# Kernel tuning notes

Measured on AMD Instinct MI355X. Metric: run time of the kernel, lower is better.

Reference implementation:

```python
import jax, jax.numpy as jnp
import numpy as np

Z, K, H, B = 32, 4, 128, 32768  # z_size, num_flows, h_size, batch


def setup_inputs() -> dict:
    key = jax.random.key(0)
    ks = jax.random.split(key, 12)
    s = 0.05  # weight scale so tanh stays in informative range
    return {
        "z0": jax.random.normal(ks[0], (B, Z), jnp.float32),
        "h": jax.random.normal(ks[1], (B, H), jnp.float32),
        "Wd": jax.random.normal(ks[2], (K * Z * Z, H), jnp.float32) * s,
        "bd": jax.random.normal(ks[3], (K * Z * Z,), jnp.float32) * s,
        "Wd1": jax.random.normal(ks[4], (K * Z, H), jnp.float32) * s,
        "bd1": jax.random.normal(ks[5], (K * Z,), jnp.float32) * s,
        "Wd2": jax.random.normal(ks[6], (K * Z, H), jnp.float32) * s,
        "bd2": jax.random.normal(ks[7], (K * Z,), jnp.float32) * s,
        "Wb": jax.random.normal(ks[8], (K * Z, H), jnp.float32) * s,
        "bb": jax.random.normal(ks[9], (K * Z,), jnp.float32) * s,
        "is_test": 0,
    }


def _encode(h, Wd, bd, Wd1, bd1, Wd2, bd2, Wb, bb):
    bsz = h.shape[0]
    full_d = (h @ Wd.T + bd).reshape(bsz, Z, Z, K)
    diag1 = jnp.tanh(h @ Wd1.T + bd1).reshape(bsz, Z, K)
    diag2 = jnp.tanh(h @ Wd2.T + bd2).reshape(bsz, Z, K)
    triu = jnp.triu(jnp.ones((Z, Z), full_d.dtype), 1)[None, :, :, None]
    eye = jnp.eye(Z, dtype=full_d.dtype)[None, :, :, None]
    # r1: strictly-upper of full_d with learned tanh diagonal; r2: transpose analog
    r1 = full_d * triu + eye * diag1[:, :, None, :]
    r2 = jnp.transpose(full_d, (0, 2, 1, 3)) * triu + eye * diag2[:, :, None, :]
    b = (h @ Wb.T + bb).reshape(bsz, Z, K)
    return r1, r2, b, diag1, diag2


def reference(z0, h, Wd, bd, Wd1, bd1, Wd2, bd2, Wb, bb, is_test):
    r1, r2, b, diag1, diag2 = _encode(h, Wd, bd, Wd1, bd1, Wd2, bd2, Wb, bb)
    z = z0
    log_det_j = jnp.zeros(z0.shape[0], z0.dtype)
    for k in range(K):
        r1k, r2k, bk = r1[..., k], r2[..., k], b[..., k]
        flip = (k % 2 == 1)  # alternate permutation (reversal) / identity
        z_per = z[:, ::-1] if flip else z
        pre = jnp.einsum('bi,bji->bj', z_per, r2k) + bk  # z_per @ r2^T + b
        t = jnp.tanh(pre)
        dz = jnp.einsum('bj,bij->bi', t, r1k)            # tanh(.) @ r1^T
        if flip:
            dz = dz[:, ::-1]
        z = z + dz
        # |det| = prod_i |1 + tanh'(pre_i) * diag_r1_i * diag_r2_i|
        diag_j = (1.0 - t * t) * (diag1[:, :, k] * diag2[:, :, k]) + 1.0
        log_det_j = log_det_j + jnp.sum(jnp.log(jnp.abs(diag_j)), axis=-1)
    return z, log_det_j
```

## Files before the change

### kernel.cpp

```cpp
#include <hip/hip_runtime.h>

typedef unsigned short ushort_t;
typedef unsigned int uint_t;
typedef __attribute__((ext_vector_type(8))) _Float16 f16x8;
typedef __attribute__((ext_vector_type(4))) _Float16 f16x4;
typedef __attribute__((ext_vector_type(4))) float floatx4;

#define ZDIM 32
#define KDIM 4
#define HDIM 128
#define B_TOTAL 32768
#define TB 64

#define WS_WD16 0
#define WS_SM16 524288

#define D_PJ 68
#define D_BI 2180
#define SH_D_OFF 0
#define AUX_PITCH 132
#define AUX_MS (64 * AUX_PITCH)
#define SH_AUX_OFF 0
#define SH_H_OFF 101376
#define SH_ZT_OFF 139520
#define SH_TT_OFF 148224
#define LDS_BYTES 152576

__device__ __forceinline__ float fast_tanh(float x) {
    float e = __expf(2.0f * x);
    return 1.0f - 2.0f / (e + 1.0f);
}
__device__ __forceinline__ float f16lo(uint_t v) {
    return (float)__builtin_bit_cast(_Float16, (ushort_t)(v & 0xFFFFu));
}
__device__ __forceinline__ float f16hi(uint_t v) {
    return (float)__builtin_bit_cast(_Float16, (ushort_t)(v >> 16));
}
__device__ __forceinline__ ushort_t f2h(float x) {
    return __builtin_bit_cast(ushort_t, (_Float16)x);
}
__device__ __forceinline__ ushort4 cvt4(float4 v) {
    ushort4 o; o.x = f2h(v.x); o.y = f2h(v.y); o.z = f2h(v.z); o.w = f2h(v.w);
    return o;
}
__device__ __forceinline__ uint2 packq(const float* p) {
    uint2 r;
    r.x = (uint_t)f2h(p[0]) | ((uint_t)f2h(p[1]) << 16);
    r.y = (uint_t)f2h(p[2]) | ((uint_t)f2h(p[3]) << 16);
    return r;
}
__device__ __forceinline__ float half_at(uint2 q, int kk) {
    uint_t w = (kk & 2) ? q.y : q.x;
    return (kk & 1) ? f16hi(w) : f16lo(w);
}

__global__ __launch_bounds__(256) void convert_kernel(
    const float* __restrict__ Wd, const float* __restrict__ Wd1,
    const float* __restrict__ Wd2, const float* __restrict__ Wb,
    ushort_t* __restrict__ ws)
{
    int g = blockIdx.x * 256 + threadIdx.x;
    if (g < 131072) {
        int k = g >> 15;
        int rem = g & 32767;
        int n = rem >> 5;
        int c4 = rem & 31;
        float4 v = *((const float4*)Wd + (size_t)(4 * n + k) * 32 + c4);
        ((ushort4*)(ws + WS_WD16))[g] = cvt4(v);
    } else {
        int s = g - 131072;
        const float* src = (s < 4096) ? Wd1 : ((s < 8192) ? Wd2 : Wb);
        int r = s & 4095;
        float4 v = ((const float4*)src)[r];
        ((ushort4*)(ws + WS_SM16))[s] = cvt4(v);
    }
}

__global__ __launch_bounds__(512, 2) void sylv_kernel(
    const ushort_t* __restrict__ wsb,
    const float* __restrict__ hglob,
    const float* __restrict__ z0,
    const float* __restrict__ bd,
    const float* __restrict__ bd1,
    const float* __restrict__ bd2,
    const float* __restrict__ bb,
    float* __restrict__ out)
{
    extern __shared__ char smem[];
    _Float16* Dh     = (_Float16*)(smem + SH_D_OFF);
    float*    sh_aux = (float*)(smem + SH_AUX_OFF);
    _Float16* sh_h   = (_Float16*)(smem + SH_H_OFF);
    float*    sh_zt  = (float*)(smem + SH_ZT_OFF);
    _Float16* Th     = (_Float16*)(smem + SH_TT_OFF);

    const int t   = threadIdx.x;
    const int bg0 = blockIdx.x * TB;
    const int lane = t & 63, w = t >> 6;
    const int l15 = lane & 15, l4 = lane >> 4;
    const int fj = t & 31;
    const int fg = t >> 5;

    {
        const float4* hsrc = (const float4*)(hglob + (size_t)bg0 * HDIM);
        #pragma unroll
        for (int it = 0; it < 4; ++it) {
            int c = t + it * 512;
            int row = c >> 5, col4 = c & 31;
            float4 v = hsrc[c];
            *(ushort4*)((ushort_t*)sh_h + row * 136 + col4 * 4) = cvt4(v);
        }
        int zb = t >> 3;
        int zi0 = (t & 7) * 4;
        float4 zv = *(const float4*)(z0 + (size_t)(bg0 + zb) * ZDIM + zi0);
        sh_zt[(zi0 + 0) * 68 + zb] = zv.x;
        sh_zt[(zi0 + 1) * 68 + zb] = zv.y;
        sh_zt[(zi0 + 2) * 68 + zb] = zv.z;
        sh_zt[(zi0 + 3) * 68 + zb] = zv.w;
    }
    __syncthreads();

    f16x8 ah[4][4];
    #pragma unroll
    for (int mt = 0; mt < 4; ++mt)
        #pragma unroll
        for (int kc = 0; kc < 4; ++kc)
            ah[mt][kc] = *(const f16x8*)(sh_h + (mt * 16 + l15) * 136 + kc * 32 + l4 * 8);

    #pragma unroll 1
    for (int pi = 0; pi < 3; ++pi) {
        int p = w * 3 + pi;
        int m_i = p >> 3, nt = p & 7, n = nt * 16 + l15;
        const _Float16* wp = (const _Float16*)(wsb + WS_SM16) + (size_t)(m_i * 128 + n) * 128 + l4 * 8;
        floatx4 a[4];
        #pragma unroll
        for (int mt = 0; mt < 4; ++mt) a[mt] = (floatx4){0.f, 0.f, 0.f, 0.f};
        #pragma unroll
        for (int kc = 0; kc < 4; ++kc) {
            f16x8 bh = *(const f16x8*)(wp + kc * 32);
            #pragma unroll
            for (int mt = 0; mt < 4; ++mt)
                a[mt] = __builtin_amdgcn_mfma_f32_16x16x32_f16(ah[mt][kc], bh, a[mt], 0, 0, 0);
        }
        const float* bv = (m_i == 0) ? bd1 : ((m_i == 1) ? bd2 : bb);
        float bias = bv[n];
        float* ap = sh_aux + m_i * AUX_MS + n;
        #pragma unroll
        for (int mt = 0; mt < 4; ++mt) {
            #pragma unroll
            for (int r = 0; r < 4; ++r) {
                float v0 = a[mt][r] + bias;
                if (m_i < 2) v0 = fast_tanh(v0);
                ap[(mt * 16 + l4 * 4 + r) * AUX_PITCH] = v0;
            }
        }
    }
    __syncthreads();

    uint2 d1q[4], d2q[4], bpq[4];
    {
        #pragma unroll
        for (int e = 0; e < 4; ++e) {
            const float* base = sh_aux + (4 * fg + e) * AUX_PITCH + 4 * fj;
            d1q[e] = packq(base + 0 * AUX_MS);
            d2q[e] = packq(base + 1 * AUX_MS);
            bpq[e] = packq(base + 2 * AUX_MS);
        }
    }
    __syncthreads();

    float ld4[4] = {0.f, 0.f, 0.f, 0.f};

    #pragma unroll 1
    for (int kk = 0; kk < KDIM; ++kk) {
        const _Float16* wdk = (const _Float16*)(wsb + WS_WD16) + (size_t)kk * 131072;
        #pragma unroll 2
        for (int g = 0; g < 8; ++g) {
            int nc = w * 128 + g * 16 + l15;
            const _Float16* w0 = wdk + (size_t)nc * 128 + l4 * 8;
            floatx4 a[4];
            #pragma unroll
            for (int mt = 0; mt < 4; ++mt) a[mt] = (floatx4){0.f, 0.f, 0.f, 0.f};
            #pragma unroll
            for (int kc = 0; kc < 4; ++kc) {
                f16x8 b0 = *(const f16x8*)(w0 + kc * 32);
                #pragma unroll
                for (int mt = 0; mt < 4; ++mt)
                    a[mt] = __builtin_amdgcn_mfma_f32_16x16x32_f16(ah[mt][kc], b0, a[mt], 0, 0, 0);
            }
            int ii = nc >> 5, jj = nc & 31;
            int base = ii * D_BI + jj * D_PJ;
            float bias0 = bd[4 * nc + kk];
            #pragma unroll
            for (int mt = 0; mt < 4; ++mt) {
                f16x4 o;
                #pragma unroll
                for (int r = 0; r < 4; ++r)
                    o[r] = (_Float16)(a[mt][r] + bias0);
                *(f16x4*)(Dh + base + mt * 16 + l4 * 4) = o;
            }
        }
        __syncthreads();

        {
            const bool flip = (kk & 1) != 0;
            const int zr_j = flip ? (31 - fj) : fj;

            float s4[4];
            {
                floatx4 zj = *(const floatx4*)(sh_zt + zr_j * 68 + 4 * fg);
                #pragma unroll
                for (int e = 0; e < 4; ++e)
                    s4[e] = half_at(bpq[e], kk) + zj[e] * half_at(d2q[e], kk);
            }
            #pragma unroll 4
            for (int i = 0; i < 32; ++i) {
                int zr_i = flip ? (31 - i) : i;
                floatx4 zi4 = *(const floatx4*)(sh_zt + zr_i * 68 + 4 * fg);
                f16x4 dd = *(const f16x4*)(Dh + i * D_BI + fj * D_PJ + 4 * fg);
                bool gt = (i > fj);
                #pragma unroll
                for (int e = 0; e < 4; ++e)
                    s4[e] = fmaf((float)dd[e], gt ? zi4[e] : 0.0f, s4[e]);
            }
            float tq4[4];
            {
                f16x4 tth;
                #pragma unroll
                for (int e = 0; e < 4; ++e) {
                    float tt = fast_tanh(s4[e]);
                    tq4[e] = tt;
                    tth[e] = (_Float16)tt;
                    float d1 = half_at(d1q[e], kk), d2 = half_at(d2q[e], kk);
                    ld4[e] += __logf(fabsf((1.f - tt * tt) * (d1 * d2) + 1.f));
                }
                *(f16x4*)(Th + fj * 68 + 4 * fg) = tth;
            }
            asm volatile("s_waitcnt lgkmcnt(0)" ::: "memory");

            float dzv4[4];
            #pragma unroll
            for (int e = 0; e < 4; ++e)
                dzv4[e] = tq4[e] * half_at(d1q[e], kk);
            #pragma unroll 4
            for (int j2 = 0; j2 < 32; ++j2) {
                f16x4 tt4 = *(const f16x4*)(Th + j2 * 68 + 4 * fg);
                f16x4 dd  = *(const f16x4*)(Dh + fj * D_BI + j2 * D_PJ + 4 * fg);
                bool gt = (j2 > fj);
                #pragma unroll
                for (int e = 0; e < 4; ++e)
                    dzv4[e] = fmaf((float)dd[e], gt ? (float)tt4[e] : 0.0f, dzv4[e]);
            }
            float* zp = sh_zt + zr_j * 68 + 4 * fg;
            floatx4 zc = *(floatx4*)zp;
            #pragma unroll
            for (int e = 0; e < 4; ++e) zc[e] += dzv4[e];
            *(floatx4*)zp = zc;
        }
        __syncthreads();
    }

    {
        floatx4 zf = *(const floatx4*)(sh_zt + fj * 68 + 4 * fg);
        #pragma unroll
        for (int e = 0; e < 4; ++e)
            out[(size_t)(bg0 + 4 * fg + e) * ZDIM + fj] = zf[e];
        #pragma unroll
        for (int e = 0; e < 4; ++e) {
            float v = ld4[e];
            v += __shfl_xor(v, 1, 32);
            v += __shfl_xor(v, 2, 32);
            v += __shfl_xor(v, 4, 32);
            v += __shfl_xor(v, 8, 32);
            v += __shfl_xor(v, 16, 32);
            if (fj == 0) out[(size_t)B_TOTAL * ZDIM + bg0 + 4 * fg + e] = v;
        }
    }
}

extern "C" void kernel_launch(void* const* d_in, const int* in_sizes, int n_in,
                              void* d_out, int out_size, void* d_ws, size_t ws_size,
                              hipStream_t stream) {
    const float* z0  = (const float*)d_in[0];
    const float* h   = (const float*)d_in[1];
    const float* Wd  = (const float*)d_in[2];
    const float* bd  = (const float*)d_in[3];
    const float* Wd1 = (const float*)d_in[4];
    const float* bd1 = (const float*)d_in[5];
    const float* Wd2 = (const float*)d_in[6];
    const float* bd2 = (const float*)d_in[7];
    const float* Wb  = (const float*)d_in[8];
    const float* bb  = (const float*)d_in[9];
    ushort_t* ws = (ushort_t*)d_ws;
    float* out = (float*)d_out;

    convert_kernel<<<560, 256, 0, stream>>>(Wd, Wd1, Wd2, Wb, ws);

    (void)hipFuncSetAttribute((const void*)sylv_kernel,
                              hipFuncAttributeMaxDynamicSharedMemorySize, LDS_BYTES);
    sylv_kernel<<<B_TOTAL / TB, 512, LDS_BYTES, stream>>>(ws, h, z0, bd, bd1, bd2, bb, out);
}
```

Before: 203.9 us.

## Double block threads and split flow reductions across half-waves

Launches 1024 threads per block instead of 512. The encoder GEMM tiles are spread over twice as many waves, and the per-flow inner reductions over i and j are split between two half-waves, combined with a cross-lane shuffle. This is meant to cut the serial latency of the flow loop per block. It risks higher register pressure under a 1024-thread launch bound and lower blocks-per-CU occupancy.

```diff
diff --git a/kernel.cpp b/kernel.cpp
--- a/kernel.cpp
+++ b/kernel.cpp
@@ -76,7 +76,7 @@
     }
 }
 
-__global__ __launch_bounds__(512, 2) void sylv_kernel(
+__global__ __launch_bounds__(1024, 1) void sylv_kernel(
     const ushort_t* __restrict__ wsb,
     const float* __restrict__ hglob,
     const float* __restrict__ z0,
@@ -95,27 +95,26 @@
 
     const int t   = threadIdx.x;
     const int bg0 = blockIdx.x * TB;
-    const int lane = t & 63, w = t >> 6;
+    const int lane = t & 63, wv = t >> 6;
     const int l15 = lane & 15, l4 = lane >> 4;
     const int fj = t & 31;
-    const int fg = t >> 5;
+    const int ih = (t >> 5) & 1;
+    const int fg = wv;
 
     {
         const float4* hsrc = (const float4*)(hglob + (size_t)bg0 * HDIM);
         #pragma unroll
-        for (int it = 0; it < 4; ++it) {
-            int c = t + it * 512;
+        for (int it = 0; it < 2; ++it) {
+            int c = t + it * 1024;
             int row = c >> 5, col4 = c & 31;
             float4 v = hsrc[c];
             *(ushort4*)((ushort_t*)sh_h + row * 136 + col4 * 4) = cvt4(v);
         }
-        int zb = t >> 3;
-        int zi0 = (t & 7) * 4;
-        float4 zv = *(const float4*)(z0 + (size_t)(bg0 + zb) * ZDIM + zi0);
+        int zb = t >> 4;
+        int zi0 = (t & 15) * 2;
+        float2 zv = *(const float2*)(z0 + (size_t)(bg0 + zb) * ZDIM + zi0);
         sh_zt[(zi0 + 0) * 68 + zb] = zv.x;
         sh_zt[(zi0 + 1) * 68 + zb] = zv.y;
-        sh_zt[(zi0 + 2) * 68 + zb] = zv.z;
-        sh_zt[(zi0 + 3) * 68 + zb] = zv.w;
     }
     __syncthreads();
 
@@ -127,30 +126,32 @@
             ah[mt][kc] = *(const f16x8*)(sh_h + (mt * 16 + l15) * 136 + kc * 32 + l4 * 8);
 
     #pragma unroll 1
-    for (int pi = 0; pi < 3; ++pi) {
-        int p = w * 3 + pi;
-        int m_i = p >> 3, nt = p & 7, n = nt * 16 + l15;
-        const _Float16* wp = (const _Float16*)(wsb + WS_SM16) + (size_t)(m_i * 128 + n) * 128 + l4 * 8;
-        floatx4 a[4];
-        #pragma unroll
-        for (int mt = 0; mt < 4; ++mt) a[mt] = (floatx4){0.f, 0.f, 0.f, 0.f};
-        #pragma unroll
-        for (int kc = 0; kc < 4; ++kc) {
-            f16x8 bh = *(const f16x8*)(wp + kc * 32);
-            #pragma unroll
-            for (int mt = 0; mt < 4; ++mt)
-                a[mt] = __builtin_amdgcn_mfma_f32_16x16x32_f16(ah[mt][kc], bh, a[mt], 0, 0, 0);
-        }
-        const float* bv = (m_i == 0) ? bd1 : ((m_i == 1) ? bd2 : bb);
-        float bias = bv[n];
-        float* ap = sh_aux + m_i * AUX_MS + n;
-        #pragma unroll
-        for (int mt = 0; mt < 4; ++mt) {
-            #pragma unroll
-            for (int r = 0; r < 4; ++r) {
-                float v0 = a[mt][r] + bias;
-                if (m_i < 2) v0 = fast_tanh(v0);
-                ap[(mt * 16 + l4 * 4 + r) * AUX_PITCH] = v0;
+    for (int pi = 0; pi < 2; ++pi) {
+        int p = wv * 2 + pi;
+        if (p < 24) {
+            int m_i = p >> 3, nt = p & 7, n = nt * 16 + l15;
+            const _Float16* wp = (const _Float16*)(wsb + WS_SM16) + (size_t)(m_i * 128 + n) * 128 + l4 * 8;
+            floatx4 a[4];
+            #pragma unroll
+            for (int mt = 0; mt < 4; ++mt) a[mt] = (floatx4){0.f, 0.f, 0.f, 0.f};
+            #pragma unroll
+            for (int kc = 0; kc < 4; ++kc) {
+                f16x8 bh = *(const f16x8*)(wp + kc * 32);
+                #pragma unroll
+                for (int mt = 0; mt < 4; ++mt)
+                    a[mt] = __builtin_amdgcn_mfma_f32_16x16x32_f16(ah[mt][kc], bh, a[mt], 0, 0, 0);
+            }
+            const float* bv = (m_i == 0) ? bd1 : ((m_i == 1) ? bd2 : bb);
+            float bias = bv[n];
+            float* ap = sh_aux + m_i * AUX_MS + n;
+            #pragma unroll
+            for (int mt = 0; mt < 4; ++mt) {
+                #pragma unroll
+                for (int r = 0; r < 4; ++r) {
+                    float v0 = a[mt][r] + bias;
+                    if (m_i < 2) v0 = fast_tanh(v0);
+                    ap[(mt * 16 + l4 * 4 + r) * AUX_PITCH] = v0;
+                }
             }
         }
     }
@@ -174,8 +175,8 @@
     for (int kk = 0; kk < KDIM; ++kk) {
         const _Float16* wdk = (const _Float16*)(wsb + WS_WD16) + (size_t)kk * 131072;
         #pragma unroll 2
-        for (int g = 0; g < 8; ++g) {
-            int nc = w * 128 + g * 16 + l15;
+        for (int g = 0; g < 4; ++g) {
+            int nc = wv * 64 + g * 16 + l15;
             const _Float16* w0 = wdk + (size_t)nc * 128 + l4 * 8;
             floatx4 a[4];
             #pragma unroll
@@ -206,14 +207,18 @@
             const int zr_j = flip ? (31 - fj) : fj;
 
             float s4[4];
-            {
+            if (ih == 0) {
                 floatx4 zj = *(const floatx4*)(sh_zt + zr_j * 68 + 4 * fg);
                 #pragma unroll
                 for (int e = 0; e < 4; ++e)
                     s4[e] = half_at(bpq[e], kk) + zj[e] * half_at(d2q[e], kk);
+            } else {
+                #pragma unroll
+                for (int e = 0; e < 4; ++e) s4[e] = 0.f;
             }
             #pragma unroll 4
-            for (int i = 0; i < 32; ++i) {
+            for (int it = 0; it < 16; ++it) {
+                int i = ih * 16 + it;
                 int zr_i = flip ? (31 - i) : i;
                 floatx4 zi4 = *(const floatx4*)(sh_zt + zr_i * 68 + 4 * fg);
                 f16x4 dd = *(const f16x4*)(Dh + i * D_BI + fj * D_PJ + 4 * fg);
@@ -222,6 +227,10 @@
                 for (int e = 0; e < 4; ++e)
                     s4[e] = fmaf((float)dd[e], gt ? zi4[e] : 0.0f, s4[e]);
             }
+            #pragma unroll
+            for (int e = 0; e < 4; ++e)
+                s4[e] += __shfl_xor(s4[e], 32, 64);
+
             float tq4[4];
             {
                 f16x4 tth;
@@ -233,16 +242,23 @@
                     float d1 = half_at(d1q[e], kk), d2 = half_at(d2q[e], kk);
                     ld4[e] += __logf(fabsf((1.f - tt * tt) * (d1 * d2) + 1.f));
                 }
-                *(f16x4*)(Th + fj * 68 + 4 * fg) = tth;
-            }
-            asm volatile("s_waitcnt lgkmcnt(0)" ::: "memory");
+                if (ih == 0)
+                    *(f16x4*)(Th + fj * 68 + 4 * fg) = tth;
+            }
+            asm volatile("" ::: "memory");
 
             float dzv4[4];
-            #pragma unroll
-            for (int e = 0; e < 4; ++e)
-                dzv4[e] = tq4[e] * half_at(d1q[e], kk);
+            if (ih == 0) {
+                #pragma unroll
+                for (int e = 0; e < 4; ++e)
+                    dzv4[e] = tq4[e] * half_at(d1q[e], kk);
+            } else {
+                #pragma unroll
+                for (int e = 0; e < 4; ++e) dzv4[e] = 0.f;
+            }
             #pragma unroll 4
-            for (int j2 = 0; j2 < 32; ++j2) {
+            for (int it = 0; it < 16; ++it) {
+                int j2 = ih * 16 + it;
                 f16x4 tt4 = *(const f16x4*)(Th + j2 * 68 + 4 * fg);
                 f16x4 dd  = *(const f16x4*)(Dh + fj * D_BI + j2 * D_PJ + 4 * fg);
                 bool gt = (j2 > fj);
@@ -250,20 +266,28 @@
                 for (int e = 0; e < 4; ++e)
                     dzv4[e] = fmaf((float)dd[e], gt ? (float)tt4[e] : 0.0f, dzv4[e]);
             }
-            float* zp = sh_zt + zr_j * 68 + 4 * fg;
-            floatx4 zc = *(floatx4*)zp;
-            #pragma unroll
-            for (int e = 0; e < 4; ++e) zc[e] += dzv4[e];
-            *(floatx4*)zp = zc;
+            #pragma unroll
+            for (int e = 0; e < 4; ++e)
+                dzv4[e] += __shfl_xor(dzv4[e], 32, 64);
+
+            if (ih == 0) {
+                float* zp = sh_zt + zr_j * 68 + 4 * fg;
+                floatx4 zc = *(floatx4*)zp;
+                #pragma unroll
+                for (int e = 0; e < 4; ++e) zc[e] += dzv4[e];
+                *(floatx4*)zp = zc;
+            }
         }
         __syncthreads();
     }
 
     {
-        floatx4 zf = *(const floatx4*)(sh_zt + fj * 68 + 4 * fg);
-        #pragma unroll
-        for (int e = 0; e < 4; ++e)
-            out[(size_t)(bg0 + 4 * fg + e) * ZDIM + fj] = zf[e];
+        if (ih == 0) {
+            floatx4 zf = *(const floatx4*)(sh_zt + fj * 68 + 4 * fg);
+            #pragma unroll
+            for (int e = 0; e < 4; ++e)
+                out[(size_t)(bg0 + 4 * fg + e) * ZDIM + fj] = zf[e];
+        }
         #pragma unroll
         for (int e = 0; e < 4; ++e) {
             float v = ld4[e];
@@ -272,7 +296,8 @@
             v += __shfl_xor(v, 4, 32);
             v += __shfl_xor(v, 8, 32);
             v += __shfl_xor(v, 16, 32);
-            if (fj == 0) out[(size_t)B_TOTAL * ZDIM + bg0 + 4 * fg + e] = v;
+            if (fj == 0 && ih == 0)
+                out[(size_t)B_TOTAL * ZDIM + bg0 + 4 * fg + e] = v;
         }
     }
 }
@@ -297,5 +322,5 @@
 
     (void)hipFuncSetAttribute((const void*)sylv_kernel,
                               hipFuncAttributeMaxDynamicSharedMemorySize, LDS_BYTES);
-    sylv_kernel<<<B_TOTAL / TB, 512, LDS_BYTES, stream>>>(ws, h, z0, bd, bd1, bd2, bb, out);
-}
+    sylv_kernel<<<B_TOTAL / TB, 1024, LDS_BYTES, stream>>>(ws, h, z0, bd, bd1, bd2, bb, out);
+}
```

New measurement: 229.0 us. 12.3% more time.

## Remap flow threads by row to skip zero triangular terms and branchless masking

Applied to the files above, without the earlier changes.

Changes the thread mapping so each wave handles four consecutive output rows (fj = t>>4). Each thread can then start its triangular loops near its own row instead of iterating over all 32 and masking with a per-element select. Only the three boundary iterations keep a mask, applied to the packed halves. Because the row→thread mapping changed, the log-det reduction moves from shuffles to a shared-memory column sum, and a full barrier replaces the lgkmcnt wait before the second product. Wave-level load imbalance across rows remains, and the extra barrier adds synchronisation.

```diff
diff --git a/kernel.cpp b/kernel.cpp
--- a/kernel.cpp
+++ b/kernel.cpp
@@ -97,8 +97,9 @@
     const int bg0 = blockIdx.x * TB;
     const int lane = t & 63, w = t >> 6;
     const int l15 = lane & 15, l4 = lane >> 4;
-    const int fj = t & 31;
-    const int fg = t >> 5;
+    const int fj = t >> 4;
+    const int fg = t & 15;
+    const int fjc = w * 4;
 
     {
         const float4* hsrc = (const float4*)(hglob + (size_t)bg0 * HDIM);
@@ -201,10 +202,10 @@
         }
         __syncthreads();
 
+        const bool flip = (kk & 1) != 0;
+        const int zr_j = flip ? (31 - fj) : fj;
+        float tq4[4];
         {
-            const bool flip = (kk & 1) != 0;
-            const int zr_j = flip ? (31 - fj) : fj;
-
             float s4[4];
             {
                 floatx4 zj = *(const floatx4*)(sh_zt + zr_j * 68 + 4 * fg);
@@ -212,43 +213,66 @@
                 for (int e = 0; e < 4; ++e)
                     s4[e] = half_at(bpq[e], kk) + zj[e] * half_at(d2q[e], kk);
             }
+            #pragma unroll
+            for (int mi = 1; mi <= 3; ++mi) {
+                int i = fjc + mi;
+                int zr_i = flip ? (31 - i) : i;
+                floatx4 zi4 = *(const floatx4*)(sh_zt + zr_i * 68 + 4 * fg);
+                uint2 du = *(const uint2*)(Dh + i * D_BI + fj * D_PJ + 4 * fg);
+                bool gt = (i > fj);
+                du.x = gt ? du.x : 0u;
+                du.y = gt ? du.y : 0u;
+                s4[0] = fmaf(f16lo(du.x), zi4[0], s4[0]);
+                s4[1] = fmaf(f16hi(du.x), zi4[1], s4[1]);
+                s4[2] = fmaf(f16lo(du.y), zi4[2], s4[2]);
+                s4[3] = fmaf(f16hi(du.y), zi4[3], s4[3]);
+            }
             #pragma unroll 4
-            for (int i = 0; i < 32; ++i) {
+            for (int i = fjc + 4; i < 32; ++i) {
                 int zr_i = flip ? (31 - i) : i;
                 floatx4 zi4 = *(const floatx4*)(sh_zt + zr_i * 68 + 4 * fg);
                 f16x4 dd = *(const f16x4*)(Dh + i * D_BI + fj * D_PJ + 4 * fg);
-                bool gt = (i > fj);
                 #pragma unroll
                 for (int e = 0; e < 4; ++e)
-                    s4[e] = fmaf((float)dd[e], gt ? zi4[e] : 0.0f, s4[e]);
-            }
-            float tq4[4];
-            {
-                f16x4 tth;
-                #pragma unroll
-                for (int e = 0; e < 4; ++e) {
-                    float tt = fast_tanh(s4[e]);
-                    tq4[e] = tt;
-                    tth[e] = (_Float16)tt;
-                    float d1 = half_at(d1q[e], kk), d2 = half_at(d2q[e], kk);
-                    ld4[e] += __logf(fabsf((1.f - tt * tt) * (d1 * d2) + 1.f));
-                }
-                *(f16x4*)(Th + fj * 68 + 4 * fg) = tth;
-            }
-            asm volatile("s_waitcnt lgkmcnt(0)" ::: "memory");
-
+                    s4[e] = fmaf((float)dd[e], zi4[e], s4[e]);
+            }
+            f16x4 tth;
+            #pragma unroll
+            for (int e = 0; e < 4; ++e) {
+                float tt = fast_tanh(s4[e]);
+                tq4[e] = tt;
+                tth[e] = (_Float16)tt;
+                float d1 = half_at(d1q[e], kk), d2 = half_at(d2q[e], kk);
+                ld4[e] += __logf(fabsf((1.f - tt * tt) * (d1 * d2) + 1.f));
+            }
+            *(f16x4*)(Th + fj * 68 + 4 * fg) = tth;
+        }
+        __syncthreads();
+        {
             float dzv4[4];
             #pragma unroll
             for (int e = 0; e < 4; ++e)
                 dzv4[e] = tq4[e] * half_at(d1q[e], kk);
+            #pragma unroll
+            for (int mi = 1; mi <= 3; ++mi) {
+                int j2 = fjc + mi;
+                uint2 tu = *(const uint2*)(Th + j2 * 68 + 4 * fg);
+                uint2 du = *(const uint2*)(Dh + fj * D_BI + j2 * D_PJ + 4 * fg);
+                bool gt = (j2 > fj);
+                du.x = gt ? du.x : 0u;
+                du.y = gt ? du.y : 0u;
+                dzv4[0] = fmaf(f16lo(du.x), f16lo(tu.x), dzv4[0]);
+                dzv4[1] = fmaf(f16hi(du.x), f16hi(tu.x), dzv4[1]);
+                dzv4[2] = fmaf(f16lo(du.y), f16lo(tu.y), dzv4[2]);
+                dzv4[3] = fmaf(f16hi(du.y), f16hi(tu.y), dzv4[3]);
+            }
             #pragma unroll 4
-            for (int j2 = 0; j2 < 32; ++j2) {
+            for (int j2 = fjc + 4; j2 < 32; ++j2) {
                 f16x4 tt4 = *(const f16x4*)(Th + j2 * 68 + 4 * fg);
                 f16x4 dd  = *(const f16x4*)(Dh + fj * D_BI + j2 * D_PJ + 4 * fg);
-                bool gt = (j2 > fj);
                 #pragma unroll
                 for (int e = 0; e < 4; ++e)
-                    dzv4[e] = fmaf((float)dd[e], gt ? (float)tt4[e] : 0.0f, dzv4[e]);
+                    dzv4[e] = fmaf((float)dd[e], (float)tt4[e], dzv4[e]);
             }
             float* zp = sh_zt + zr_j * 68 + 4 * fg;
             floatx4 zc = *(floatx4*)zp;
@@ -264,15 +288,19 @@
         #pragma unroll
         for (int e = 0; e < 4; ++e)
             out[(size_t)(bg0 + 4 * fg + e) * ZDIM + fj] = zf[e];
-        #pragma unroll
-        for (int e = 0; e < 4; ++e) {
-            float v = ld4[e];
-            v += __shfl_xor(v, 1, 32);
-            v += __shfl_xor(v, 2, 32);
-            v += __shfl_xor(v, 4, 32);
-            v += __shfl_xor(v, 8, 32);
-            v += __shfl_xor(v, 16, 32);
-            if (fj == 0) out[(size_t)B_TOTAL * ZDIM + bg0 + 4 * fg + e] = v;
+
+        float* lsc = (float*)smem;
+        floatx4 lv;
+        #pragma unroll
+        for (int e = 0; e < 4; ++e) lv[e] = ld4[e];
+        *(floatx4*)(lsc + fj * 68 + 4 * fg) = lv;
+        __syncthreads();
+        if (t < 64) {
+            float v = 0.f;
+            #pragma unroll 8
+            for (int j = 0; j < 32; ++j)
+                v += lsc[j * 68 + t];
+            out[(size_t)B_TOTAL * ZDIM + bg0 + t] = v;
         }
     }
 }
```

After: 197.6 us. 3.1% less time.
